# Performance work log

Hardware: AMD Instinct MI355X
Metric: run time of the kernel (lower is better)

Reference implementation:

```python
import jax, jax.numpy as jnp
import numpy as np

IN_FEATURES = 4096
OUT_FEATURES = 16384


def setup_inputs() -> dict:
    key = jax.random.key(0)
    kx, kw = jax.random.split(key)
    x = jax.random.normal(kx, (8, 2048, IN_FEATURES), dtype=jnp.float32)
    # reset_parameters: uniform(-1.5, 1.5)
    weight = jax.random.uniform(kw, (OUT_FEATURES, IN_FEATURES), dtype=jnp.float32,
                                minval=-1.5, maxval=1.5)
    weight_scale = jnp.ones((1,), dtype=jnp.float32)
    return {"x": x, "weight": weight, "weight_scale": weight_scale}


def reference(x, weight, weight_scale):
    # Ternary quantization: threshold = 0.7 * mean(|W|); W_q = sign(W) * (|W| > thr)
    abs_w = jnp.abs(weight)
    threshold = 0.7 * abs_w.mean()
    weight_q = jnp.sign(weight) * (abs_w > threshold).astype(weight.dtype)
    weight_q = weight_q * weight_scale  # broadcast scalar scale
    # F.linear: x @ W_q^T  -> [B, S, out_features]
    out = jnp.einsum('bsi,oi->bso', x, weight_q)
    return out
```

## Files before the change

### kernel.cpp

```cpp
#include <hip/hip_runtime.h>
#include <hip/hip_bf16.h>
#include <stdint.h>


typedef __attribute__((ext_vector_type(4))) int i32x4;
typedef __attribute__((ext_vector_type(8))) unsigned short u16x8;

#define M_ROWS 16384
#define K_DIM  4096
#define N_DIM  16384

#define RED_BLOCKS 2048

__global__ void absum_part_kernel(const float4* __restrict__ W4,
                                  double* __restrict__ part, long long n4) {
  double s = 0.0;
  const long long stride = (long long)gridDim.x * blockDim.x;
  for (long long i = (long long)blockIdx.x * blockDim.x + threadIdx.x; i < n4; i += stride) {
    float4 v = W4[i];
    s += (double)fabsf(v.x);
    s += (double)fabsf(v.y);
    s += (double)fabsf(v.z);
    s += (double)fabsf(v.w);
  }
  for (int o = 32; o > 0; o >>= 1) s += __shfl_down(s, o, 64);
  __shared__ double p[4];
  if ((threadIdx.x & 63) == 0) p[threadIdx.x >> 6] = s;
  __syncthreads();
  if (threadIdx.x == 0) part[blockIdx.x] = p[0] + p[1] + p[2] + p[3];
}

__global__ void reduce_sum_kernel(const double* __restrict__ part,
                                  double* __restrict__ sum, int n) {
  double s = 0.0;
  for (int i = threadIdx.x; i < n; i += blockDim.x) s += part[i];
  for (int o = 32; o > 0; o >>= 1) s += __shfl_down(s, o, 64);
  __shared__ double p[4];
  if ((threadIdx.x & 63) == 0) p[threadIdx.x >> 6] = s;
  __syncthreads();
  if (threadIdx.x == 0) *sum = p[0] + p[1] + p[2] + p[3];
}

__device__ __forceinline__ int tern_i8(float w, float thr) {
  return ((fabsf(w) > thr) ? ((w > 0.0f) ? 1 : -1) : 0) & 255;
}

__global__ void quant_w_kernel(const float4* __restrict__ W4,
                               signed char* __restrict__ Wq,
                               const double* __restrict__ sum_ptr, long long n16) {
  const double mean = *sum_ptr / (double)((long long)N_DIM * K_DIM);
  const float thr = (float)(0.7 * mean);
  const long long stride = (long long)gridDim.x * blockDim.x;
  for (long long i = (long long)blockIdx.x * blockDim.x + threadIdx.x; i < n16; i += stride) {
    float4 a = W4[4 * i], b = W4[4 * i + 1], c = W4[4 * i + 2], d = W4[4 * i + 3];
    int4 o;
    o.x = tern_i8(a.x, thr) | (tern_i8(a.y, thr) << 8) |
          (tern_i8(a.z, thr) << 16) | (tern_i8(a.w, thr) << 24);
    o.y = tern_i8(b.x, thr) | (tern_i8(b.y, thr) << 8) |
          (tern_i8(b.z, thr) << 16) | (tern_i8(b.w, thr) << 24);
    o.z = tern_i8(c.x, thr) | (tern_i8(c.y, thr) << 8) |
          (tern_i8(c.z, thr) << 16) | (tern_i8(c.w, thr) << 24);
    o.w = tern_i8(d.x, thr) | (tern_i8(d.y, thr) << 8) |
          (tern_i8(d.z, thr) << 16) | (tern_i8(d.w, thr) << 24);
    *(int4*)(Wq + i * 16) = o;
  }
}

__global__ void quant_x_kernel(const float4* __restrict__ X4,
                               signed char* __restrict__ Xq,
                               float* __restrict__ xs) {
  const int row = blockIdx.x;
  const int t = threadIdx.x;
  const float4* src = X4 + (size_t)row * (K_DIM / 4);
  float4 v[4];
#pragma unroll
  for (int i = 0; i < 4; ++i) v[i] = src[i * 256 + t];
  float m = 0.f;
#pragma unroll
  for (int i = 0; i < 4; ++i) {
    m = fmaxf(m, fabsf(v[i].x)); m = fmaxf(m, fabsf(v[i].y));
    m = fmaxf(m, fabsf(v[i].z)); m = fmaxf(m, fabsf(v[i].w));
  }
  for (int o = 32; o > 0; o >>= 1) m = fmaxf(m, __shfl_down(m, o, 64));
  __shared__ float p[4];
  if ((t & 63) == 0) p[t >> 6] = m;
  __syncthreads();
  const float bm = fmaxf(fmaxf(p[0], p[1]), fmaxf(p[2], p[3]));
  const float inv = (bm > 0.f) ? 127.0f / bm : 0.f;
  if (t == 0) xs[row] = (bm > 0.f) ? bm / 127.0f : 0.f;
  int* dst = (int*)(Xq + (size_t)row * K_DIM);
#pragma unroll
  for (int i = 0; i < 4; ++i) {
    const int q0 = __float2int_rn(v[i].x * inv) & 255;
    const int q1 = __float2int_rn(v[i].y * inv) & 255;
    const int q2 = __float2int_rn(v[i].z * inv) & 255;
    const int q3 = __float2int_rn(v[i].w * inv) & 255;
    dst[i * 256 + t] = q0 | (q1 << 8) | (q2 << 16) | (q3 << 24);
  }
}

#define BM 256
#define BN 256
#define BK 64
#define NT (K_DIM / BK)

__global__ __launch_bounds__(512, 2) void gemm_bt_kernel(
    const signed char* __restrict__ A,
    const signed char* __restrict__ B,
    float* __restrict__ C,
    const float* __restrict__ xs,
    const float* __restrict__ scale_ptr) {
  constexpr int K = K_DIM, N = N_DIM;
  __shared__ __align__(16) signed char lds[4][2][BM][BK];

  const int tid = threadIdx.x;
  const int wave = tid >> 6;
  const int lane = tid & 63;

  const int x = blockIdx.x & 7;
  const int l = blockIdx.x >> 3;
  const int g = l >> 5;
  const int s = l & 31;
  const int bm = g * 4 + (s & 3);
  const int bn = x * 8 + (s >> 2);

  const int wr = wave >> 2;
  const int wc = wave & 3;

  const signed char* Ag = A + (size_t)(bm * BM) * K;
  const signed char* Bg = B + (size_t)(bn * BN) * K;

  const int strow = lane >> 2;
  const int scol = ((((lane & 3) - (lane >> 3)) & 3) << 4);

  const int frow = lane & 15;
  const int fsw = ((((lane >> 4) + ((lane & 15) >> 1)) & 3) << 4);

#define STAGE(u)                                                                     \
  {                                                                                  \
    const int kk0_ = (u) * BK;                                                       \
    signed char* Ab_ = &lds[(u) & 3][0][0][0];                                       \
    signed char* Bb_ = &lds[(u) & 3][1][0][0];                                       \
    _Pragma("unroll")                                                                \
    for (int i_ = 0; i_ < 2; ++i_) {                                                 \
      const int ch_ = wave * 2 + i_;                                                 \
      const int row_ = ch_ * 16 + strow;                                             \
      __builtin_amdgcn_global_load_lds(                                              \
          (__attribute__((address_space(1))) void*)(Ag + (size_t)row_ * K + kk0_ + scol), \
          (__attribute__((address_space(3))) void*)(Ab_ + ch_ * 16 * BK), 16, 0, 0); \
      __builtin_amdgcn_global_load_lds(                                              \
          (__attribute__((address_space(1))) void*)(Bg + (size_t)row_ * K + kk0_ + scol), \
          (__attribute__((address_space(3))) void*)(Bb_ + ch_ * 16 * BK), 16, 0, 0); \
    }                                                                                \
  }

#define RD_B(P, n_) (*(const i32x4*)((P) + (wc * 64 + (n_) * 16 + frow) * BK + fsw))
#define RD_A(P, m_) (*(const i32x4*)((P) + (wr * 128 + (m_) * 16 + frow) * BK + fsw))

#define MF4(m_, CA, CB)                                                              \
  {                                                                                  \
    _Pragma("unroll")                                                                \
    for (int n_ = 0; n_ < 4; ++n_)                                                   \
      acc[m_][n_] = __builtin_amdgcn_mfma_i32_16x16x64_i8(CA[m_], CB[n_],            \
                                                          acc[m_][n_], 0, 0, 0);     \
  }

#define SB __builtin_amdgcn_sched_barrier(0)

#define ITER(T, CA, CB, NA, NB, RD)                                                  \
  {                                                                                  \
    if ((T) + 3 < NT) STAGE((T) + 3);                                                \
    SB;                                                                              \
    if ((T) < NT - 3) {                                                              \
      asm volatile("s_waitcnt vmcnt(8)" ::: "memory");                               \
    } else if ((T) == NT - 3) {                                                      \
      asm volatile("s_waitcnt vmcnt(4)" ::: "memory");                               \
    } else if ((T) == NT - 2) {                                                      \
      asm volatile("s_waitcnt vmcnt(0)" ::: "memory");                               \
    }                                                                                \
    __builtin_amdgcn_s_barrier();                                                    \
    SB;                                                                              \
    const signed char* NAp_ = &lds[((T) + 1) & 3][0][0][0];                          \
    const signed char* NBp_ = &lds[((T) + 1) & 3][1][0][0];                          \
    __builtin_amdgcn_s_setprio(1);                                                   \
    MF4(0, CA, CB);                                                                  \
    SB;                                                                              \
    if (RD) { NB[0] = RD_B(NBp_, 0); NB[1] = RD_B(NBp_, 1); }                        \
    SB;                                                                              \
    MF4(1, CA, CB);                                                                  \
    SB;                                                                              \
    if (RD) { NB[2] = RD_B(NBp_, 2); NB[3] = RD_B(NBp_, 3); }                        \
    SB;                                                                              \
    MF4(2, CA, CB);                                                                  \
    SB;                                                                              \
    if (RD) { NA[0] = RD_A(NAp_, 0); NA[1] = RD_A(NAp_, 1); }                        \
    SB;                                                                              \
    MF4(3, CA, CB);                                                                  \
    SB;                                                                              \
    if (RD) { NA[2] = RD_A(NAp_, 2); NA[3] = RD_A(NAp_, 3); }                        \
    SB;                                                                              \
    MF4(4, CA, CB);                                                                  \
    SB;                                                                              \
    if (RD) { NA[4] = RD_A(NAp_, 4); NA[5] = RD_A(NAp_, 5); }                        \
    SB;                                                                              \
    MF4(5, CA, CB);                                                                  \
    SB;                                                                              \
    if (RD) { NA[6] = RD_A(NAp_, 6); NA[7] = RD_A(NAp_, 7); }                        \
    SB;                                                                              \
    MF4(6, CA, CB);                                                                  \
    MF4(7, CA, CB);                                                                  \
    __builtin_amdgcn_s_setprio(0);                                                   \
    SB;                                                                              \
  }

  i32x4 acc[8][4] = {};
  i32x4 af0[8], bf0[4], af1[8], bf1[4];

  STAGE(0);
  STAGE(1);
  STAGE(2);
  asm volatile("s_waitcnt vmcnt(8)" ::: "memory");
  __builtin_amdgcn_s_barrier();
  SB;
#pragma unroll
  for (int n = 0; n < 4; ++n) bf0[n] = RD_B(&lds[0][1][0][0], n);
#pragma unroll
  for (int m = 0; m < 8; ++m) af0[m] = RD_A(&lds[0][0][0][0], m);
  SB;

  for (int t = 0; t < NT - 2; t += 2) {
    ITER(t, af0, bf0, af1, bf1, 1);
    ITER(t + 1, af1, bf1, af0, bf0, 1);
  }
  ITER(NT - 2, af0, bf0, af1, bf1, 1);
  ITER(NT - 1, af1, bf1, af0, bf0, 0);
#undef ITER
#undef SB
#undef MF4
#undef RD_A
#undef RD_B
#undef STAGE

  const float wscale = *scale_ptr;
  const int crow0 = bm * BM + wr * 128;
  const int ccol0 = bn * BN + wc * 64;
#pragma unroll
  for (int m = 0; m < 8; ++m)
#pragma unroll
    for (int j = 0; j < 4; ++j) {
      const int row = crow0 + m * 16 + ((lane >> 4) << 2) + j;
      const float sc = xs[row] * wscale;
#pragma unroll
      for (int n = 0; n < 4; ++n) {
        const int col = ccol0 + n * 16 + (lane & 15);
        C[(size_t)row * N + col] = (float)acc[m][n][j] * sc;
      }
    }
}

extern "C" void kernel_launch(void* const* d_in, const int* in_sizes, int n_in,
                              void* d_out, int out_size, void* d_ws, size_t ws_size,
                              hipStream_t stream) {
  (void)in_sizes; (void)n_in; (void)out_size; (void)ws_size;
  const float* x = (const float*)d_in[0];
  const float* w = (const float*)d_in[1];
  const float* scale = (const float*)d_in[2];
  float* out = (float*)d_out;

  char* ws = (char*)d_ws;
  double* part = (double*)ws;
  double* sum = (double*)(ws + 16384);
  float* xs = (float*)(ws + 32768);
  signed char* Wq = (signed char*)(ws + 98304);
  signed char* Xq = (signed char*)(ws + 98304 + (size_t)N_DIM * K_DIM);

  const long long nW = (long long)N_DIM * K_DIM;

  absum_part_kernel<<<RED_BLOCKS, 256, 0, stream>>>((const float4*)w, part, nW / 4);
  reduce_sum_kernel<<<1, 256, 0, stream>>>(part, sum, RED_BLOCKS);
  quant_w_kernel<<<2048, 256, 0, stream>>>((const float4*)w, Wq, sum, nW / 16);
  quant_x_kernel<<<M_ROWS, 256, 0, stream>>>((const float4*)x, Xq, xs);

  const int nblocks = (M_ROWS / BM) * (N_DIM / BN);
  gemm_bt_kernel<<<nblocks, 512, 0, stream>>>(Xq, Wq, out, xs, scale);
}
```

Before: 1.221 ms.

## Replace 4-stage LDS pipeline with simple double-buffered loop

```diff
diff --git a/kernel.cpp b/kernel.cpp
--- a/kernel.cpp
+++ b/kernel.cpp
@@ -4,7 +4,6 @@
 
 
 typedef __attribute__((ext_vector_type(4))) int i32x4;
-typedef __attribute__((ext_vector_type(8))) unsigned short u16x8;
 
 #define M_ROWS 16384
 #define K_DIM  4096
@@ -111,7 +110,7 @@
     const float* __restrict__ xs,
     const float* __restrict__ scale_ptr) {
   constexpr int K = K_DIM, N = N_DIM;
-  __shared__ __align__(16) signed char lds[4][2][BM][BK];
+  __shared__ __align__(16) signed char lds[2][2][BM][BK];
 
   const int tid = threadIdx.x;
   const int wave = tid >> 6;
@@ -136,11 +135,11 @@
   const int frow = lane & 15;
   const int fsw = ((((lane >> 4) + ((lane & 15) >> 1)) & 3) << 4);
 
-#define STAGE(u)                                                                     \
+#define STAGE(u, bi)                                                                 \
   {                                                                                  \
     const int kk0_ = (u) * BK;                                                       \
-    signed char* Ab_ = &lds[(u) & 3][0][0][0];                                       \
-    signed char* Bb_ = &lds[(u) & 3][1][0][0];                                       \
+    signed char* Ab_ = &lds[bi][0][0][0];                                            \
+    signed char* Bb_ = &lds[bi][1][0][0];                                            \
     _Pragma("unroll")                                                                \
     for (int i_ = 0; i_ < 2; ++i_) {                                                 \
       const int ch_ = wave * 2 + i_;                                                 \
@@ -154,89 +153,51 @@
     }                                                                                \
   }
 
-#define RD_B(P, n_) (*(const i32x4*)((P) + (wc * 64 + (n_) * 16 + frow) * BK + fsw))
-#define RD_A(P, m_) (*(const i32x4*)((P) + (wr * 128 + (m_) * 16 + frow) * BK + fsw))
-
-#define MF4(m_, CA, CB)                                                              \
+#define RD_B(bi, n_) \
+  (*(const i32x4*)(&lds[bi][1][wc * 64 + (n_) * 16 + frow][0] + fsw))
+#define RD_A(bi, m_) \
+  (*(const i32x4*)(&lds[bi][0][wr * 128 + (m_) * 16 + frow][0] + fsw))
+
+#define SB __builtin_amdgcn_sched_barrier(0)
+
+#define ITER(T, BI)                                                                  \
   {                                                                                  \
-    _Pragma("unroll")                                                                \
-    for (int n_ = 0; n_ < 4; ++n_)                                                   \
-      acc[m_][n_] = __builtin_amdgcn_mfma_i32_16x16x64_i8(CA[m_], CB[n_],            \
-                                                          acc[m_][n_], 0, 0, 0);     \
-  }
-
-#define SB __builtin_amdgcn_sched_barrier(0)
-
-#define ITER(T, CA, CB, NA, NB, RD)                                                  \
-  {                                                                                  \
-    if ((T) + 3 < NT) STAGE((T) + 3);                                                \
+    if ((T) + 1 < NT) STAGE((T) + 1, BI ^ 1);                                        \
     SB;                                                                              \
-    if ((T) < NT - 3) {                                                              \
-      asm volatile("s_waitcnt vmcnt(8)" ::: "memory");                               \
-    } else if ((T) == NT - 3) {                                                      \
-      asm volatile("s_waitcnt vmcnt(4)" ::: "memory");                               \
-    } else if ((T) == NT - 2) {                                                      \
-      asm volatile("s_waitcnt vmcnt(0)" ::: "memory");                               \
-    }                                                                                \
-    __builtin_amdgcn_s_barrier();                                                    \
-    SB;                                                                              \
-    const signed char* NAp_ = &lds[((T) + 1) & 3][0][0][0];                          \
-    const signed char* NBp_ = &lds[((T) + 1) & 3][1][0][0];                          \
+    i32x4 af[8], bf[4];                                                              \
+    _Pragma("unroll")                                                                \
+    for (int n_ = 0; n_ < 4; ++n_) bf[n_] = RD_B(BI, n_);                            \
+    _Pragma("unroll")                                                                \
+    for (int m_ = 0; m_ < 8; ++m_) af[m_] = RD_A(BI, m_);                            \
     __builtin_amdgcn_s_setprio(1);                                                   \
-    MF4(0, CA, CB);                                                                  \
-    SB;                                                                              \
-    if (RD) { NB[0] = RD_B(NBp_, 0); NB[1] = RD_B(NBp_, 1); }                        \
-    SB;                                                                              \
-    MF4(1, CA, CB);                                                                  \
-    SB;                                                                              \
-    if (RD) { NB[2] = RD_B(NBp_, 2); NB[3] = RD_B(NBp_, 3); }                        \
-    SB;                                                                              \
-    MF4(2, CA, CB);                                                                  \
-    SB;                                                                              \
-    if (RD) { NA[0] = RD_A(NAp_, 0); NA[1] = RD_A(NAp_, 1); }                        \
-    SB;                                                                              \
-    MF4(3, CA, CB);                                                                  \
-    SB;                                                                              \
-    if (RD) { NA[2] = RD_A(NAp_, 2); NA[3] = RD_A(NAp_, 3); }                        \
-    SB;                                                                              \
-    MF4(4, CA, CB);                                                                  \
-    SB;                                                                              \
-    if (RD) { NA[4] = RD_A(NAp_, 4); NA[5] = RD_A(NAp_, 5); }                        \
-    SB;                                                                              \
-    MF4(5, CA, CB);                                                                  \
-    SB;                                                                              \
-    if (RD) { NA[6] = RD_A(NAp_, 6); NA[7] = RD_A(NAp_, 7); }                        \
-    SB;                                                                              \
-    MF4(6, CA, CB);                                                                  \
-    MF4(7, CA, CB);                                                                  \
+    _Pragma("unroll")                                                                \
+    for (int m_ = 0; m_ < 8; ++m_)                                                   \
+      _Pragma("unroll")                                                              \
+      for (int n_ = 0; n_ < 4; ++n_)                                                 \
+        acc[m_][n_] = __builtin_amdgcn_mfma_i32_16x16x64_i8(af[m_], bf[n_],          \
+                                                            acc[m_][n_], 0, 0, 0);   \
     __builtin_amdgcn_s_setprio(0);                                                   \
     SB;                                                                              \
+    if ((T) + 1 < NT) {                                                              \
+      asm volatile("s_waitcnt vmcnt(0)" ::: "memory");                               \
+      __builtin_amdgcn_s_barrier();                                                  \
+    }                                                                                \
+    SB;                                                                              \
   }
 
   i32x4 acc[8][4] = {};
-  i32x4 af0[8], bf0[4], af1[8], bf1[4];
-
-  STAGE(0);
-  STAGE(1);
-  STAGE(2);
-  asm volatile("s_waitcnt vmcnt(8)" ::: "memory");
+
+  STAGE(0, 0);
+  asm volatile("s_waitcnt vmcnt(0)" ::: "memory");
   __builtin_amdgcn_s_barrier();
   SB;
-#pragma unroll
-  for (int n = 0; n < 4; ++n) bf0[n] = RD_B(&lds[0][1][0][0], n);
-#pragma unroll
-  for (int m = 0; m < 8; ++m) af0[m] = RD_A(&lds[0][0][0][0], m);
-  SB;
-
-  for (int t = 0; t < NT - 2; t += 2) {
-    ITER(t, af0, bf0, af1, bf1, 1);
-    ITER(t + 1, af1, bf1, af0, bf0, 1);
-  }
-  ITER(NT - 2, af0, bf0, af1, bf1, 1);
-  ITER(NT - 1, af1, bf1, af0, bf0, 0);
+
+  for (int t = 0; t < NT; t += 2) {
+    ITER(t, 0);
+    ITER(t + 1, 1);
+  }
 #undef ITER
 #undef SB
-#undef MF4
 #undef RD_A
 #undef RD_B
 #undef STAGE
```

Measured after the change: 1.373 ms. +12.4%, slower.
